# Optimization experiments

Measured on AMD Instinct MI355X. Metric: run time of the kernel, lower is better.

Reference implementation:

```python
import jax, jax.numpy as jnp
import numpy as np

N_NODES = 100000
N_EDGES = 1600000
D_FEAT = 256
HID = 128
DEG_DIM = 128  # data.degree_exist_matrix.shape[1]


def setup_inputs() -> dict:
    key = jax.random.key(0)
    ks = jax.random.split(key, 12)
    s = lambda fan_in: 1.0 / np.sqrt(fan_in)
    x = jax.random.normal(ks[0], (N_NODES, D_FEAT), dtype=jnp.float32)
    edge_index = jax.random.randint(ks[1], (2, N_EDGES), 0, N_NODES, dtype=jnp.int32)
    return {
        "x": x,
        "edge_index": edge_index,
        # GCNConv 1 / 2 (PyG stores weight [in,out], bias [out])
        "W1": jax.random.uniform(ks[2], (D_FEAT, HID), jnp.float32, -s(D_FEAT), s(D_FEAT)),
        "b1": jnp.zeros((HID,), jnp.float32),
        "W2": jax.random.uniform(ks[3], (HID, HID), jnp.float32, -s(HID), s(HID)),
        "b2": jnp.zeros((HID,), jnp.float32),
        # down_sample Linear(D_FEAT, HID)
        "Wd": jax.random.uniform(ks[4], (D_FEAT, HID), jnp.float32, -s(D_FEAT), s(D_FEAT)),
        "bd": jax.random.uniform(ks[5], (HID,), jnp.float32, -s(D_FEAT), s(D_FEAT)),
        # linear2: Degree_layer(HID, 1) ~ Linear(HID, 1)
        "Wdeg": jax.random.uniform(ks[6], (HID, 1), jnp.float32, -s(HID), s(HID)),
        "bdeg": jax.random.uniform(ks[7], (1,), jnp.float32, -s(HID), s(HID)),
        # linear3: Linear(HID, DEG_DIM)
        "W3": jax.random.uniform(ks[8], (HID, DEG_DIM), jnp.float32, -s(HID), s(HID)),
        "b3": jax.random.uniform(ks[9], (DEG_DIM,), jnp.float32, -s(HID), s(HID)),
    }


def gcn_conv(x, W, b, src, dst, n):
    """PyG GCNConv: D^-1/2 (A+I) D^-1/2 X W + b (symmetric norm, self-loops)."""
    h = x @ W  # [N, out]
    deg = jax.ops.segment_sum(jnp.ones_like(dst, dtype=h.dtype), dst, num_segments=n) + 1.0
    dinv = jax.lax.rsqrt(deg)  # deg >= 1 from self loop
    coef = dinv[src] * dinv[dst]  # [E]
    msgs = h[src] * coef[:, None]  # [E, out] -- dominant gather
    agg = jax.ops.segment_sum(msgs, dst, num_segments=n)
    agg = agg + h * (dinv * dinv)[:, None]  # self-loop contribution
    return agg + b


def reference(x, edge_index, W1, b1, W2, b2, Wd, bd, Wdeg, bdeg, W3, b3):
    n = x.shape[0]
    src, dst = edge_index[0], edge_index[1]
    original_x = x @ Wd + bd
    h = gcn_conv(x, W1, b1, src, dst, n)
    h = jax.nn.relu(h)  # dropout is identity in eval mode
    h = gcn_conv(h, W2, b2, src, dst, n)
    h = h + original_x  # residual
    result1 = jax.nn.log_softmax(h, axis=-1)        # [N, HID]
    result2 = (h @ Wdeg + bdeg).squeeze(-1)          # [N]
    result3 = h @ W3 + b3                            # [N, DEG_DIM]
    return (result1, result2, result3)
```

## Files before the change

kernel.cpp:

```cpp
#include <hip/hip_runtime.h>


typedef __attribute__((ext_vector_type(8))) short bf16x8;
typedef __attribute__((ext_vector_type(4))) float f32x4;

#define CDIV(a, b) (((a) + (b) - 1) / (b))

#define GLOBAL_AS __attribute__((address_space(1)))
#define LDS_AS __attribute__((address_space(3)))

__device__ __forceinline__ void gload16(const void* g, void* l) {
  __builtin_amdgcn_global_load_lds((const GLOBAL_AS unsigned int*)g,
                                   (LDS_AS unsigned int*)l, 16, 0, 0);
}

__device__ __forceinline__ float b2f(unsigned short u) {
  union { unsigned int i; float f; } x; x.i = ((unsigned int)u) << 16; return x.f;
}
__device__ __forceinline__ unsigned short f2b(float f) {
  union { float f; unsigned int i; } x; x.f = f;
  unsigned int r = x.i + 0x7fffu + ((x.i >> 16) & 1u);
  return (unsigned short)(r >> 16);
}
__device__ __forceinline__ float rlf(float v, int j) {
  union { float f; int i; } x; x.f = v;
  x.i = __builtin_amdgcn_readlane(x.i, j);
  return x.f;
}


__global__ void k_wtrans4(const float* __restrict__ W1, const float* __restrict__ Wd,
                          const float* __restrict__ W2, const float* __restrict__ W3,
                          unsigned short* __restrict__ W1t, unsigned short* __restrict__ Wdt,
                          unsigned short* __restrict__ W2t, unsigned short* __restrict__ W3t) {
  int idx = blockIdx.x * blockDim.x + threadIdx.x;
  const float* in; unsigned short* out; int K, N;
  if (idx < 32768)       { in = W1; out = W1t; K = 256; N = 128; }
  else if (idx < 65536)  { in = Wd; out = Wdt; K = 256; N = 128; idx -= 32768; }
  else if (idx < 81920)  { in = W2; out = W2t; K = 128; N = 128; idx -= 65536; }
  else if (idx < 98304)  { in = W3; out = W3t; K = 128; N = 128; idx -= 81920; }
  else return;
  int k = idx / N, n = idx - k * N;
  out[n * K + k] = f2b(in[idx]);
}

__global__ void k_scan1(const int* __restrict__ deg, int* __restrict__ lscan,
                        int* __restrict__ partials, float* __restrict__ dinv, int n) {
  __shared__ int sd[256];
  int tid = threadIdx.x;
  int base = blockIdx.x * 2048 + tid * 8;
  int v[8]; int tsum = 0;
#pragma unroll
  for (int i = 0; i < 8; ++i) {
    int idx = base + i;
    int xv = (idx < n) ? deg[idx] : 0;
    v[i] = xv; tsum += xv;
    if (idx < n) dinv[idx] = 1.0f / sqrtf((float)xv + 1.0f);
  }
  sd[tid] = tsum;
  __syncthreads();
  for (int off = 1; off < 256; off <<= 1) {
    int t = (tid >= off) ? sd[tid - off] : 0;
    __syncthreads();
    sd[tid] += t;
    __syncthreads();
  }
  int run = sd[tid] - tsum;
#pragma unroll
  for (int i = 0; i < 8; ++i) {
    int idx = base + i;
    if (idx < n) lscan[idx] = run;
    run += v[i];
  }
  if (tid == 255) partials[blockIdx.x] = sd[255];
}

__global__ void k_scan2(const int* __restrict__ partials, int* __restrict__ pprefix, int nb) {
  if (threadIdx.x == 0 && blockIdx.x == 0) {
    int run = 0;
    for (int i = 0; i < nb; ++i) { pprefix[i] = run; run += partials[i]; }
    pprefix[nb] = run;
  }
}

__global__ void k_scan3(const int* __restrict__ pprefix, int* row_start,
                        int* __restrict__ cursor, int n, int E) {
  int idx = blockIdx.x * blockDim.x + threadIdx.x;
  if (idx >= n) return;
  int v = row_start[idx] + pprefix[idx >> 11];
  row_start[idx] = v;
  cursor[idx] = v;
  if (idx == 0) row_start[n] = E;
}


#define BIN_CHUNK 4096
#define OVF_CAP 65536

__global__ __launch_bounds__(256) void k_binA(
    const int* __restrict__ ei, int E, int nbuck, int cap,
    int* __restrict__ deg, int2* __restrict__ pairs, int* __restrict__ bcnt,
    int2* __restrict__ ovf, int* __restrict__ ovf_cnt) {
  __shared__ int lcnt[256];
  __shared__ int lbase[256];
  int tid = threadIdx.x;
  for (int i = tid; i < nbuck; i += 256) lcnt[i] = 0;
  __syncthreads();
  int base_e = blockIdx.x * BIN_CHUNK;
  int src[16], dst[16], lofs[16];
#pragma unroll
  for (int i = 0; i < 16; ++i) {
    int e = base_e + i * 256 + tid;
    if (e < E) {
      int s = ei[e], d = ei[E + e];
      src[i] = s; dst[i] = d;
      atomicAdd(&deg[d], 1);
      lofs[i] = atomicAdd(&lcnt[d >> 9], 1);
    } else {
      dst[i] = -1;
    }
  }
  __syncthreads();
  for (int b = tid; b < nbuck; b += 256)
    lbase[b] = atomicAdd(&bcnt[b], lcnt[b]);
  __syncthreads();
#pragma unroll
  for (int i = 0; i < 16; ++i) {
    if (dst[i] < 0) continue;
    int b = dst[i] >> 9;
    int gpos = lbase[b] + lofs[i];
    if (gpos < cap) {
      pairs[(size_t)b * cap + gpos] = make_int2(src[i], dst[i]);
    } else {
      int op = atomicAdd(ovf_cnt, 1);
      if (op < OVF_CAP) ovf[op] = make_int2(src[i], dst[i]);
    }
  }
}

__global__ __launch_bounds__(256) void k_binB(
    const int2* __restrict__ pairs, const int* __restrict__ bcnt,
    int nbuck, int cap,
    const int2* __restrict__ ovf, const int* __restrict__ ovf_cnt,
    int* __restrict__ cursor, int* __restrict__ csr_src) {
  if ((int)blockIdx.x < nbuck) {
    int b = blockIdx.x;
    int cnt = bcnt[b]; if (cnt > cap) cnt = cap;
    const int2* p = pairs + (size_t)b * cap;
    for (int i = threadIdx.x; i < cnt; i += 256) {
      int2 e = p[i];
      int pos = atomicAdd(&cursor[e.y], 1);
      csr_src[pos] = e.x;
    }
  } else {
    int total = *ovf_cnt; if (total > OVF_CAP) total = OVF_CAP;
    int start = (blockIdx.x - nbuck) * 256 + threadIdx.x;
    for (int i = start; i < total; i += 8 * 256) {
      int2 e = ovf[i];
      int pos = atomicAdd(&cursor[e.y], 1);
      csr_src[pos] = e.x;
    }
  }
}


__global__ __launch_bounds__(512) void k_gemm_x2(
    const float* __restrict__ X,
    const unsigned short* __restrict__ B1t,
    const unsigned short* __restrict__ B2t,
    const float* __restrict__ bias2,
    unsigned short* __restrict__ O1, float* __restrict__ O2, int n) {
  __shared__ char lds[65536];
  const int flat = threadIdx.x;
  const int wave = flat >> 6, lane = flat & 63;
  const int l15 = lane & 15, q = lane >> 4;
  const int wM = wave >> 1, wN = wave & 1;
  const int rowBase = blockIdx.x * 128;
  const int colBase = wN * 64;

  auto stage = [&](int kb, int buf) {
    char* ldsA = lds + buf * 32768;
    char* ldsB = ldsA + 16384;
    const char* Xb = (const char*)X;
#pragma unroll
    for (int j = 0; j < 2; ++j) {
      int i = j * 512 + flat;
      int row = i >> 3, pslot = i & 7;
      int lslot = pslot ^ (row & 7);
      int rowc = rowBase + row; if (rowc >= n) rowc = n - 1;
      gload16(Xb + (size_t)rowc * 1024 + (size_t)(kb * 128 + lslot * 16),
              ldsA + (j * 512 + wave * 64) * 16);
    }
#pragma unroll
    for (int j = 0; j < 2; ++j) {
      int i = j * 512 + flat;
      int col = i >> 3, pslot = i & 7;
      int lslot = pslot ^ (col & 7);
      const char* src = (lslot >= 4) ? (const char*)B2t : (const char*)B1t;
      gload16(src + (size_t)col * 512 + kb * 64 + (lslot & 3) * 16,
              ldsB + (j * 512 + wave * 64) * 16);
    }
  };

  f32x4 acc1[2][4], acc2[2][4];
#pragma unroll
  for (int i = 0; i < 2; ++i)
#pragma unroll
    for (int j = 0; j < 4; ++j) {
      acc1[i][j] = (f32x4){0.f, 0.f, 0.f, 0.f};
      acc2[i][j] = (f32x4){0.f, 0.f, 0.f, 0.f};
    }

  stage(0, 0);
  __syncthreads();

#pragma unroll
  for (int kb = 0; kb < 8; ++kb) {
    int cur = kb & 1;
    if (kb < 7) stage(kb + 1, cur ^ 1);
    char* ldsA = lds + cur * 32768;
    char* ldsB = ldsA + 16384;
    bf16x8 a[2], b1v[4], b2v[4];
#pragma unroll
    for (int mt = 0; mt < 2; ++mt) {
      int row = wM * 32 + mt * 16 + l15;
      uint4 lo = *(const uint4*)(ldsA + row * 128 + (((2 * q) ^ (row & 7)) * 16));
      uint4 hi = *(const uint4*)(ldsA + row * 128 + (((2 * q + 1) ^ (row & 7)) * 16));
      union { bf16x8 v; unsigned int u[4]; } r;
      r.u[0] = __builtin_amdgcn_perm(lo.y + 0x8000u, lo.x + 0x8000u, 0x07060302u);
      r.u[1] = __builtin_amdgcn_perm(lo.w + 0x8000u, lo.z + 0x8000u, 0x07060302u);
      r.u[2] = __builtin_amdgcn_perm(hi.y + 0x8000u, hi.x + 0x8000u, 0x07060302u);
      r.u[3] = __builtin_amdgcn_perm(hi.w + 0x8000u, hi.z + 0x8000u, 0x07060302u);
      a[mt] = r.v;
    }
#pragma unroll
    for (int nt = 0; nt < 4; ++nt) {
      int col = colBase + nt * 16 + l15;
      b1v[nt] = *(const bf16x8*)(ldsB + col * 128 + ((q ^ (col & 7)) * 16));
      b2v[nt] = *(const bf16x8*)(ldsB + col * 128 + (((4 + q) ^ (col & 7)) * 16));
    }
#pragma unroll
    for (int mt = 0; mt < 2; ++mt)
#pragma unroll
      for (int nt = 0; nt < 4; ++nt) {
        acc1[mt][nt] = __builtin_amdgcn_mfma_f32_16x16x32_bf16(a[mt], b1v[nt], acc1[mt][nt], 0, 0, 0);
        acc2[mt][nt] = __builtin_amdgcn_mfma_f32_16x16x32_bf16(a[mt], b2v[nt], acc2[mt][nt], 0, 0, 0);
      }
    __syncthreads();
  }

#pragma unroll
  for (int mt = 0; mt < 2; ++mt)
#pragma unroll
    for (int nt = 0; nt < 4; ++nt) {
      int col = colBase + nt * 16 + l15;
      float bb = bias2[col];
#pragma unroll
      for (int r = 0; r < 4; ++r) {
        int row = rowBase + wM * 32 + mt * 16 + q * 4 + r;
        if (row < n) {
          O1[(size_t)row * 128 + col] = f2b(acc1[mt][nt][r]);
          O2[(size_t)row * 128 + col] = acc2[mt][nt][r] + bb;
        }
      }
    }
}

template <int OUT_F32>
__global__ __launch_bounds__(512) void k_gemm_h(
    const unsigned short* __restrict__ X, const unsigned short* __restrict__ Bt,
    const float* __restrict__ bias, unsigned short* __restrict__ Ob,
    float* __restrict__ Of, int n) {
  __shared__ char lds[65536];
  const int flat = threadIdx.x;
  const int wave = flat >> 6, lane = flat & 63;
  const int l15 = lane & 15, q = lane >> 4;
  const int wM = wave >> 1, wN = wave & 1;
  const int rowBase = blockIdx.x * 128;
  const int colBase = wN * 64;

  auto stage = [&](int ks, int buf) {
    char* ldsA = lds + buf * 32768;
    char* ldsB = ldsA + 16384;
#pragma unroll
    for (int j = 0; j < 2; ++j) {
      int i = j * 512 + flat;
      int row = i >> 3, pslot = i & 7;
      int lslot = pslot ^ (row & 7);
      int rowc = rowBase + row; if (rowc >= n) rowc = n - 1;
      gload16((const char*)X + (size_t)rowc * 256 + ks * 128 + lslot * 16,
              ldsA + (j * 512 + wave * 64) * 16);
    }
#pragma unroll
    for (int j = 0; j < 2; ++j) {
      int i = j * 512 + flat;
      int col = i >> 3, pslot = i & 7;
      int lslot = pslot ^ (col & 7);
      gload16((const char*)Bt + (size_t)col * 256 + ks * 128 + lslot * 16,
              ldsB + (j * 512 + wave * 64) * 16);
    }
  };

  f32x4 acc[2][4];
#pragma unroll
  for (int i = 0; i < 2; ++i)
#pragma unroll
    for (int j = 0; j < 4; ++j) acc[i][j] = (f32x4){0.f, 0.f, 0.f, 0.f};

  stage(0, 0);
  __syncthreads();
  stage(1, 1);

#pragma unroll
  for (int ks = 0; ks < 2; ++ks) {
    char* ldsA = lds + ks * 32768;
    char* ldsB = ldsA + 16384;
#pragma unroll
    for (int k2 = 0; k2 < 2; ++k2) {
      bf16x8 a[2], b[4];
#pragma unroll
      for (int mt = 0; mt < 2; ++mt) {
        int row = wM * 32 + mt * 16 + l15;
        a[mt] = *(const bf16x8*)(ldsA + row * 128 + (((k2 * 4 + q) ^ (row & 7)) * 16));
      }
#pragma unroll
      for (int nt = 0; nt < 4; ++nt) {
        int col = colBase + nt * 16 + l15;
        b[nt] = *(const bf16x8*)(ldsB + col * 128 + (((k2 * 4 + q) ^ (col & 7)) * 16));
      }
#pragma unroll
      for (int mt = 0; mt < 2; ++mt)
#pragma unroll
        for (int nt = 0; nt < 4; ++nt)
          acc[mt][nt] = __builtin_amdgcn_mfma_f32_16x16x32_bf16(a[mt], b[nt], acc[mt][nt], 0, 0, 0);
    }
    if (ks == 0) __syncthreads();
  }

#pragma unroll
  for (int mt = 0; mt < 2; ++mt)
#pragma unroll
    for (int nt = 0; nt < 4; ++nt) {
      int col = colBase + nt * 16 + l15;
      float bb = OUT_F32 ? bias[col] : 0.f;
#pragma unroll
      for (int r = 0; r < 4; ++r) {
        int row = rowBase + wM * 32 + mt * 16 + q * 4 + r;
        if (row < n) {
          if (OUT_F32) Of[(size_t)row * 128 + col] = acc[mt][nt][r] + bb;
          else Ob[(size_t)row * 128 + col] = f2b(acc[mt][nt][r]);
        }
      }
    }
}


__device__ __forceinline__ void agg_edges(
    const unsigned short* __restrict__ h, const int* __restrict__ csr_src,
    const float* __restrict__ dinv, int beg, int end, int lane,
    float& a0, float& a1) {
  for (int base = beg; base < end; base += 64) {
    int m = end - base; if (m > 64) m = 64;
    int ok = (base + lane < end);
    int idx_l = ok ? csr_src[base + lane] : 0;
    float c_l = ok ? dinv[idx_l] : 0.f;
    int j = 0;
    for (; j + 3 < m; j += 4) {
      int s0 = __builtin_amdgcn_readlane(idx_l, j);
      int s1 = __builtin_amdgcn_readlane(idx_l, j + 1);
      int s2 = __builtin_amdgcn_readlane(idx_l, j + 2);
      int s3 = __builtin_amdgcn_readlane(idx_l, j + 3);
      float c0 = rlf(c_l, j), c1 = rlf(c_l, j + 1);
      float c2 = rlf(c_l, j + 2), c3 = rlf(c_l, j + 3);
      unsigned int v0 = *(const unsigned int*)(h + (size_t)s0 * 128 + lane * 2);
      unsigned int v1 = *(const unsigned int*)(h + (size_t)s1 * 128 + lane * 2);
      unsigned int v2 = *(const unsigned int*)(h + (size_t)s2 * 128 + lane * 2);
      unsigned int v3 = *(const unsigned int*)(h + (size_t)s3 * 128 + lane * 2);
      a0 += c0 * b2f((unsigned short)v0); a1 += c0 * b2f((unsigned short)(v0 >> 16));
      a0 += c1 * b2f((unsigned short)v1); a1 += c1 * b2f((unsigned short)(v1 >> 16));
      a0 += c2 * b2f((unsigned short)v2); a1 += c2 * b2f((unsigned short)(v2 >> 16));
      a0 += c3 * b2f((unsigned short)v3); a1 += c3 * b2f((unsigned short)(v3 >> 16));
    }
    for (; j < m; ++j) {
      int s = __builtin_amdgcn_readlane(idx_l, j);
      float c = rlf(c_l, j);
      unsigned int v = *(const unsigned int*)(h + (size_t)s * 128 + lane * 2);
      a0 += c * b2f((unsigned short)v);
      a1 += c * b2f((unsigned short)(v >> 16));
    }
  }
}

__global__ __launch_bounds__(256) void k_agg1(
    const unsigned short* __restrict__ h,
    const int* __restrict__ row_start, const int* __restrict__ csr_src,
    const float* __restrict__ dinv,
    const float* __restrict__ bias,
    unsigned short* __restrict__ hout, int n) {
  int gw = blockIdx.x * (blockDim.x >> 6) + (threadIdx.x >> 6);
  int lane = threadIdx.x & 63;
  if (gw >= n) return;
  int beg = row_start[gw], end = row_start[gw + 1];
  float dg = dinv[gw];
  float a0 = 0.f, a1 = 0.f;
  agg_edges(h, csr_src, dinv, beg, end, lane, a0, a1);
  a0 *= dg; a1 *= dg;
  float sc = dg * dg;
  unsigned int v = *(const unsigned int*)(h + (size_t)gw * 128 + lane * 2);
  a0 += sc * b2f((unsigned short)v);
  a1 += sc * b2f((unsigned short)(v >> 16));
  a0 += bias[lane * 2];
  a1 += bias[lane * 2 + 1];
  a0 = fmaxf(a0, 0.f);
  a1 = fmaxf(a1, 0.f);
  unsigned int o = (unsigned int)f2b(a0) | ((unsigned int)f2b(a1) << 16);
  *(unsigned int*)(hout + (size_t)gw * 128 + lane * 2) = o;
}

__global__ __launch_bounds__(256) void k_agg2_epi(
    const unsigned short* __restrict__ h,
    const int* __restrict__ row_start, const int* __restrict__ csr_src,
    const float* __restrict__ dinv,
    const float* __restrict__ bias,
    float* res_out1,
    const float* __restrict__ wdeg, const float* __restrict__ bdeg,
    float* __restrict__ out2,
    unsigned short* __restrict__ hf,
    int n) {
  int gw = blockIdx.x * (blockDim.x >> 6) + (threadIdx.x >> 6);
  int lane = threadIdx.x & 63;
  if (gw >= n) return;
  int beg = row_start[gw], end = row_start[gw + 1];
  float dg = dinv[gw];
  float a0 = 0.f, a1 = 0.f;
  agg_edges(h, csr_src, dinv, beg, end, lane, a0, a1);
  a0 *= dg; a1 *= dg;
  float sc = dg * dg;
  unsigned int v = *(const unsigned int*)(h + (size_t)gw * 128 + lane * 2);
  a0 += sc * b2f((unsigned short)v);
  a1 += sc * b2f((unsigned short)(v >> 16));
  a0 += bias[lane * 2];
  a1 += bias[lane * 2 + 1];
  float2 rv = *(const float2*)(res_out1 + (size_t)gw * 128 + lane * 2);
  a0 += rv.x;
  a1 += rv.y;
  unsigned int o = (unsigned int)f2b(a0) | ((unsigned int)f2b(a1) << 16);
  *(unsigned int*)(hf + (size_t)gw * 128 + lane * 2) = o;
  float t = a0 * wdeg[lane * 2] + a1 * wdeg[lane * 2 + 1];
#pragma unroll
  for (int m = 32; m >= 1; m >>= 1) t += __shfl_xor(t, m);
  if (lane == 0) out2[gw] = t + bdeg[0];
  float mx = fmaxf(a0, a1);
#pragma unroll
  for (int m = 32; m >= 1; m >>= 1) mx = fmaxf(mx, __shfl_xor(mx, m));
  float l = __expf(a0 - mx) + __expf(a1 - mx);
#pragma unroll
  for (int m = 32; m >= 1; m >>= 1) l += __shfl_xor(l, m);
  float ls = mx + __logf(l);
  float2 o1; o1.x = a0 - ls; o1.y = a1 - ls;
  *(float2*)(res_out1 + (size_t)gw * 128 + lane * 2) = o1;
}


extern "C" void kernel_launch(void* const* d_in, const int* in_sizes, int n_in,
                              void* d_out, int out_size, void* d_ws, size_t ws_size,
                              hipStream_t stream) {
  const float* x   = (const float*)d_in[0];
  const int*   ei  = (const int*)d_in[1];
  const float* W1  = (const float*)d_in[2];
  const float* b1  = (const float*)d_in[3];
  const float* W2  = (const float*)d_in[4];
  const float* b2  = (const float*)d_in[5];
  const float* Wd  = (const float*)d_in[6];
  const float* bd  = (const float*)d_in[7];
  const float* Wdg = (const float*)d_in[8];
  const float* bdg = (const float*)d_in[9];
  const float* W3  = (const float*)d_in[10];
  const float* b3  = (const float*)d_in[11];

  const int N = in_sizes[0] / 256;
  const int E = in_sizes[1] / 2;

  char* w = (char*)d_ws;
  auto alloc = [&](size_t bytes) {
    char* p = w;
    w += (bytes + 255) & ~(size_t)255;
    return p;
  };
  unsigned short* W1t  = (unsigned short*)alloc((size_t)256 * 128 * 2);
  unsigned short* Wdt  = (unsigned short*)alloc((size_t)256 * 128 * 2);
  unsigned short* W2t  = (unsigned short*)alloc((size_t)128 * 128 * 2);
  unsigned short* W3t  = (unsigned short*)alloc((size_t)128 * 128 * 2);
  unsigned short* bufC = (unsigned short*)alloc((size_t)N * 128 * 2);
  int*   deg      = (int*)alloc((size_t)N * 4);
  float* dinv     = (float*)alloc((size_t)N * 4);
  int*   row_start= (int*)alloc((size_t)(N + 1) * 4);
  int*   cursor   = (int*)alloc((size_t)N * 4);
  int*   partials = (int*)alloc(4096);
  int*   pprefix  = (int*)alloc(4096);
  int*   csr_src  = (int*)alloc((size_t)E * 4);
  int*   bcnt     = (int*)alloc(2048);
  int*   ovf_cnt  = bcnt + 256;
  int2*  ovf      = (int2*)alloc((size_t)OVF_CAP * 8);

  float* out1 = (float*)d_out;
  float* out2 = out1 + (size_t)N * 128;
  float* out3 = out2 + (size_t)N;
  unsigned short* bufA = (unsigned short*)out3;

  const int nbuck = CDIV(N, 512);
  int cap = (E / nbuck) + (E / nbuck) / 2;
  cap = (cap + 255) & ~255;
  size_t bufC_bytes = (size_t)N * 128 * 2;
  if ((size_t)nbuck * cap * 8 > bufC_bytes)
    cap = (int)(bufC_bytes / ((size_t)nbuck * 8));
  int2* pairs = (int2*)bufC;

  hipMemsetAsync(deg, 0, (size_t)N * 4, stream);
  hipMemsetAsync(bcnt, 0, 2048, stream);

  k_wtrans4<<<CDIV(98304, 256), 256, 0, stream>>>(W1, Wd, W2, W3, W1t, Wdt, W2t, W3t);

  k_binA<<<CDIV(E, BIN_CHUNK), 256, 0, stream>>>(ei, E, nbuck, cap, deg, pairs,
                                                 bcnt, ovf, ovf_cnt);

  k_gemm_x2<<<CDIV(N, 128), 512, 0, stream>>>(x, W1t, Wdt, bd, bufA, out1, N);

  const int nb = CDIV(N, 2048);
  k_scan1<<<nb, 256, 0, stream>>>(deg, row_start, partials, dinv, N);
  k_scan2<<<1, 64, 0, stream>>>(partials, pprefix, nb);
  k_scan3<<<CDIV(N, 256), 256, 0, stream>>>(pprefix, row_start, cursor, N, E);

  k_binB<<<nbuck + 8, 256, 0, stream>>>(pairs, bcnt, nbuck, cap, ovf, ovf_cnt,
                                        cursor, csr_src);

  k_agg1<<<CDIV(N, 4), 256, 0, stream>>>(bufA, row_start, csr_src, dinv, b1, bufC, N);

  k_gemm_h<0><<<CDIV(N, 128), 512, 0, stream>>>(bufC, W2t, nullptr, bufA, nullptr, N);

  k_agg2_epi<<<CDIV(N, 4), 256, 0, stream>>>(bufA, row_start, csr_src, dinv,
                                             b2, out1, Wdg, bdg, out2, bufC, N);

  k_gemm_h<1><<<CDIV(N, 128), 512, 0, stream>>>(bufC, W3t, b3, nullptr, out3, N);
}
```

Baseline: 534.7 us.

## Pre-scale GEMM outputs by dinv and gather edges with 16-byte loads

The source-side normalisation dinv[src] is folded into the GEMM epilogues, so the aggregation kernels gather pre-scaled rows and only add them. This removes the per-edge dinv gather and multiply. The edge loop now splits a wave into four 16-lane groups, each loading a full 256-byte row with uint4 loads on a different edge, then reduces across groups with shuffles. The first GEMM moves after the degree scan so dinv exists when it runs, which removes its overlap with the scan. The change also adds nontemporal stores and a cheaper bf16 pack, and pads dinv so the float4 reads past N stay in bounds.

```diff
diff --git a/kernel.cpp b/kernel.cpp
--- a/kernel.cpp
+++ b/kernel.cpp
@@ -22,10 +22,14 @@
   unsigned int r = x.i + 0x7fffu + ((x.i >> 16) & 1u);
   return (unsigned short)(r >> 16);
 }
-__device__ __forceinline__ float rlf(float v, int j) {
-  union { float f; int i; } x; x.f = v;
-  x.i = __builtin_amdgcn_readlane(x.i, j);
-  return x.f;
+__device__ __forceinline__ void add2(float& a0, float& a1, unsigned int u) {
+  union { unsigned int i; float f; } lo, hi;
+  lo.i = u << 16; hi.i = u & 0xffff0000u;
+  a0 += lo.f; a1 += hi.f;
+}
+__device__ __forceinline__ unsigned int pack2(float lo, float hi) {
+  return __builtin_amdgcn_perm(__float_as_uint(hi) + 0x8000u,
+                               __float_as_uint(lo) + 0x8000u, 0x07060302u);
 }
 
 
@@ -169,6 +173,7 @@
     const unsigned short* __restrict__ B1t,
     const unsigned short* __restrict__ B2t,
     const float* __restrict__ bias2,
+    const float* __restrict__ dinvp,
     unsigned short* __restrict__ O1, float* __restrict__ O2, int n) {
   __shared__ char lds[65536];
   const int flat = threadIdx.x;
@@ -250,7 +255,8 @@
   }
 
 #pragma unroll
-  for (int mt = 0; mt < 2; ++mt)
+  for (int mt = 0; mt < 2; ++mt) {
+    float4 dv = *(const float4*)(dinvp + rowBase + wM * 32 + mt * 16 + q * 4);
 #pragma unroll
     for (int nt = 0; nt < 4; ++nt) {
       int col = colBase + nt * 16 + l15;
@@ -259,18 +265,20 @@
       for (int r = 0; r < 4; ++r) {
         int row = rowBase + wM * 32 + mt * 16 + q * 4 + r;
         if (row < n) {
-          O1[(size_t)row * 128 + col] = f2b(acc1[mt][nt][r]);
+          float dvr = (r == 0) ? dv.x : (r == 1) ? dv.y : (r == 2) ? dv.z : dv.w;
+          O1[(size_t)row * 128 + col] = f2b(acc1[mt][nt][r] * dvr);
           O2[(size_t)row * 128 + col] = acc2[mt][nt][r] + bb;
         }
       }
     }
+  }
 }
 
 template <int OUT_F32>
 __global__ __launch_bounds__(512) void k_gemm_h(
     const unsigned short* __restrict__ X, const unsigned short* __restrict__ Bt,
-    const float* __restrict__ bias, unsigned short* __restrict__ Ob,
-    float* __restrict__ Of, int n) {
+    const float* __restrict__ bias, const float* __restrict__ dinvp,
+    unsigned short* __restrict__ Ob, float* __restrict__ Of, int n) {
   __shared__ char lds[65536];
   const int flat = threadIdx.x;
   const int wave = flat >> 6, lane = flat & 63;
@@ -338,7 +346,9 @@
   }
 
 #pragma unroll
-  for (int mt = 0; mt < 2; ++mt)
+  for (int mt = 0; mt < 2; ++mt) {
+    float4 dv;
+    if (!OUT_F32) dv = *(const float4*)(dinvp + rowBase + wM * 32 + mt * 16 + q * 4);
 #pragma unroll
     for (int nt = 0; nt < 4; ++nt) {
       int col = colBase + nt * 16 + l15;
@@ -347,47 +357,59 @@
       for (int r = 0; r < 4; ++r) {
         int row = rowBase + wM * 32 + mt * 16 + q * 4 + r;
         if (row < n) {
-          if (OUT_F32) Of[(size_t)row * 128 + col] = acc[mt][nt][r] + bb;
-          else Ob[(size_t)row * 128 + col] = f2b(acc[mt][nt][r]);
+          if (OUT_F32) {
+            __builtin_nontemporal_store(acc[mt][nt][r] + bb, &Of[(size_t)row * 128 + col]);
+          } else {
+            float dvr = (r == 0) ? dv.x : (r == 1) ? dv.y : (r == 2) ? dv.z : dv.w;
+            Ob[(size_t)row * 128 + col] = f2b(acc[mt][nt][r] * dvr);
+          }
         }
       }
     }
-}
-
-
-__device__ __forceinline__ void agg_edges(
+  }
+}
+
+
+__device__ __forceinline__ void agg_edges4(
     const unsigned short* __restrict__ h, const int* __restrict__ csr_src,
-    const float* __restrict__ dinv, int beg, int end, int lane,
-    float& a0, float& a1) {
+    int beg, int end, int lane, int grp, int sub, float* acc) {
   for (int base = beg; base < end; base += 64) {
     int m = end - base; if (m > 64) m = 64;
-    int ok = (base + lane < end);
-    int idx_l = ok ? csr_src[base + lane] : 0;
-    float c_l = ok ? dinv[idx_l] : 0.f;
-    int j = 0;
-    for (; j + 3 < m; j += 4) {
-      int s0 = __builtin_amdgcn_readlane(idx_l, j);
-      int s1 = __builtin_amdgcn_readlane(idx_l, j + 1);
-      int s2 = __builtin_amdgcn_readlane(idx_l, j + 2);
-      int s3 = __builtin_amdgcn_readlane(idx_l, j + 3);
-      float c0 = rlf(c_l, j), c1 = rlf(c_l, j + 1);
-      float c2 = rlf(c_l, j + 2), c3 = rlf(c_l, j + 3);
-      unsigned int v0 = *(const unsigned int*)(h + (size_t)s0 * 128 + lane * 2);
-      unsigned int v1 = *(const unsigned int*)(h + (size_t)s1 * 128 + lane * 2);
-      unsigned int v2 = *(const unsigned int*)(h + (size_t)s2 * 128 + lane * 2);
-      unsigned int v3 = *(const unsigned int*)(h + (size_t)s3 * 128 + lane * 2);
-      a0 += c0 * b2f((unsigned short)v0); a1 += c0 * b2f((unsigned short)(v0 >> 16));
-      a0 += c1 * b2f((unsigned short)v1); a1 += c1 * b2f((unsigned short)(v1 >> 16));
-      a0 += c2 * b2f((unsigned short)v2); a1 += c2 * b2f((unsigned short)(v2 >> 16));
-      a0 += c3 * b2f((unsigned short)v3); a1 += c3 * b2f((unsigned short)(v3 >> 16));
-    }
-    for (; j < m; ++j) {
-      int s = __builtin_amdgcn_readlane(idx_l, j);
-      float c = rlf(c_l, j);
-      unsigned int v = *(const unsigned int*)(h + (size_t)s * 128 + lane * 2);
-      a0 += c * b2f((unsigned short)v);
-      a1 += c * b2f((unsigned short)(v >> 16));
-    }
+    int idx_l = (base + lane < end) ? csr_src[base + lane] : 0;
+    for (int j = 0; j < m; j += 16) {
+      int s0 = __builtin_amdgcn_ds_bpermute((j + grp) << 2, idx_l);
+      int s1 = __builtin_amdgcn_ds_bpermute((j + 4 + grp) << 2, idx_l);
+      int s2 = __builtin_amdgcn_ds_bpermute((j + 8 + grp) << 2, idx_l);
+      int s3 = __builtin_amdgcn_ds_bpermute((j + 12 + grp) << 2, idx_l);
+      uint4 v0 = *(const uint4*)(h + (size_t)s0 * 128 + sub * 8);
+      uint4 v1 = *(const uint4*)(h + (size_t)s1 * 128 + sub * 8);
+      uint4 v2 = *(const uint4*)(h + (size_t)s2 * 128 + sub * 8);
+      uint4 v3 = *(const uint4*)(h + (size_t)s3 * 128 + sub * 8);
+      if (j + grp < m) {
+        add2(acc[0], acc[1], v0.x); add2(acc[2], acc[3], v0.y);
+        add2(acc[4], acc[5], v0.z); add2(acc[6], acc[7], v0.w);
+      }
+      if (j + 4 + grp < m) {
+        add2(acc[0], acc[1], v1.x); add2(acc[2], acc[3], v1.y);
+        add2(acc[4], acc[5], v1.z); add2(acc[6], acc[7], v1.w);
+      }
+      if (j + 8 + grp < m) {
+        add2(acc[0], acc[1], v2.x); add2(acc[2], acc[3], v2.y);
+        add2(acc[4], acc[5], v2.z); add2(acc[6], acc[7], v2.w);
+      }
+      if (j + 12 + grp < m) {
+        add2(acc[0], acc[1], v3.x); add2(acc[2], acc[3], v3.y);
+        add2(acc[4], acc[5], v3.z); add2(acc[6], acc[7], v3.w);
+      }
+    }
+  }
+}
+
+__device__ __forceinline__ void grp_reduce(float* acc) {
+#pragma unroll
+  for (int i = 0; i < 8; ++i) {
+    acc[i] += __shfl_xor(acc[i], 16);
+    acc[i] += __shfl_xor(acc[i], 32);
   }
 }
 
@@ -397,24 +419,31 @@
     const float* __restrict__ dinv,
     const float* __restrict__ bias,
     unsigned short* __restrict__ hout, int n) {
-  int gw = blockIdx.x * (blockDim.x >> 6) + (threadIdx.x >> 6);
+  int gw = blockIdx.x * 4 + (threadIdx.x >> 6);
   int lane = threadIdx.x & 63;
+  int grp = lane >> 4, sub = lane & 15;
   if (gw >= n) return;
   int beg = row_start[gw], end = row_start[gw + 1];
-  float dg = dinv[gw];
-  float a0 = 0.f, a1 = 0.f;
-  agg_edges(h, csr_src, dinv, beg, end, lane, a0, a1);
-  a0 *= dg; a1 *= dg;
-  float sc = dg * dg;
-  unsigned int v = *(const unsigned int*)(h + (size_t)gw * 128 + lane * 2);
-  a0 += sc * b2f((unsigned short)v);
-  a1 += sc * b2f((unsigned short)(v >> 16));
-  a0 += bias[lane * 2];
-  a1 += bias[lane * 2 + 1];
-  a0 = fmaxf(a0, 0.f);
-  a1 = fmaxf(a1, 0.f);
-  unsigned int o = (unsigned int)f2b(a0) | ((unsigned int)f2b(a1) << 16);
-  *(unsigned int*)(hout + (size_t)gw * 128 + lane * 2) = o;
+  float acc[8] = {0.f, 0.f, 0.f, 0.f, 0.f, 0.f, 0.f, 0.f};
+  agg_edges4(h, csr_src, beg, end, lane, grp, sub, acc);
+  grp_reduce(acc);
+  if (grp == 0) {
+    float dg = dinv[gw];
+    uint4 sv = *(const uint4*)(h + (size_t)gw * 128 + sub * 8);
+    add2(acc[0], acc[1], sv.x); add2(acc[2], acc[3], sv.y);
+    add2(acc[4], acc[5], sv.z); add2(acc[6], acc[7], sv.w);
+    float4 b0 = *(const float4*)(bias + sub * 8);
+    float4 b1v = *(const float4*)(bias + sub * 8 + 4);
+    float a[8];
+    a[0] = fmaxf(acc[0] * dg + b0.x, 0.f); a[1] = fmaxf(acc[1] * dg + b0.y, 0.f);
+    a[2] = fmaxf(acc[2] * dg + b0.z, 0.f); a[3] = fmaxf(acc[3] * dg + b0.w, 0.f);
+    a[4] = fmaxf(acc[4] * dg + b1v.x, 0.f); a[5] = fmaxf(acc[5] * dg + b1v.y, 0.f);
+    a[6] = fmaxf(acc[6] * dg + b1v.z, 0.f); a[7] = fmaxf(acc[7] * dg + b1v.w, 0.f);
+    uint4 o;
+    o.x = pack2(a[0], a[1]); o.y = pack2(a[2], a[3]);
+    o.z = pack2(a[4], a[5]); o.w = pack2(a[6], a[7]);
+    *(uint4*)(hout + (size_t)gw * 128 + sub * 8) = o;
+  }
 }
 
 __global__ __launch_bounds__(256) void k_agg2_epi(
@@ -427,38 +456,55 @@
     float* __restrict__ out2,
     unsigned short* __restrict__ hf,
     int n) {
-  int gw = blockIdx.x * (blockDim.x >> 6) + (threadIdx.x >> 6);
+  int gw = blockIdx.x * 4 + (threadIdx.x >> 6);
   int lane = threadIdx.x & 63;
+  int grp = lane >> 4, sub = lane & 15;
   if (gw >= n) return;
   int beg = row_start[gw], end = row_start[gw + 1];
-  float dg = dinv[gw];
-  float a0 = 0.f, a1 = 0.f;
-  agg_edges(h, csr_src, dinv, beg, end, lane, a0, a1);
-  a0 *= dg; a1 *= dg;
-  float sc = dg * dg;
-  unsigned int v = *(const unsigned int*)(h + (size_t)gw * 128 + lane * 2);
-  a0 += sc * b2f((unsigned short)v);
-  a1 += sc * b2f((unsigned short)(v >> 16));
-  a0 += bias[lane * 2];
-  a1 += bias[lane * 2 + 1];
-  float2 rv = *(const float2*)(res_out1 + (size_t)gw * 128 + lane * 2);
-  a0 += rv.x;
-  a1 += rv.y;
-  unsigned int o = (unsigned int)f2b(a0) | ((unsigned int)f2b(a1) << 16);
-  *(unsigned int*)(hf + (size_t)gw * 128 + lane * 2) = o;
-  float t = a0 * wdeg[lane * 2] + a1 * wdeg[lane * 2 + 1];
-#pragma unroll
-  for (int m = 32; m >= 1; m >>= 1) t += __shfl_xor(t, m);
-  if (lane == 0) out2[gw] = t + bdeg[0];
-  float mx = fmaxf(a0, a1);
-#pragma unroll
-  for (int m = 32; m >= 1; m >>= 1) mx = fmaxf(mx, __shfl_xor(mx, m));
-  float l = __expf(a0 - mx) + __expf(a1 - mx);
-#pragma unroll
-  for (int m = 32; m >= 1; m >>= 1) l += __shfl_xor(l, m);
-  float ls = mx + __logf(l);
-  float2 o1; o1.x = a0 - ls; o1.y = a1 - ls;
-  *(float2*)(res_out1 + (size_t)gw * 128 + lane * 2) = o1;
+  float acc[8] = {0.f, 0.f, 0.f, 0.f, 0.f, 0.f, 0.f, 0.f};
+  agg_edges4(h, csr_src, beg, end, lane, grp, sub, acc);
+  grp_reduce(acc);
+  if (grp == 0) {
+    float dg = dinv[gw];
+    uint4 sv = *(const uint4*)(h + (size_t)gw * 128 + sub * 8);
+    add2(acc[0], acc[1], sv.x); add2(acc[2], acc[3], sv.y);
+    add2(acc[4], acc[5], sv.z); add2(acc[6], acc[7], sv.w);
+    float4 b0 = *(const float4*)(bias + sub * 8);
+    float4 b1v = *(const float4*)(bias + sub * 8 + 4);
+    float4 r0 = *(const float4*)(res_out1 + (size_t)gw * 128 + sub * 8);
+    float4 r1 = *(const float4*)(res_out1 + (size_t)gw * 128 + sub * 8 + 4);
+    float a[8];
+    a[0] = acc[0] * dg + b0.x + r0.x; a[1] = acc[1] * dg + b0.y + r0.y;
+    a[2] = acc[2] * dg + b0.z + r0.z; a[3] = acc[3] * dg + b0.w + r0.w;
+    a[4] = acc[4] * dg + b1v.x + r1.x; a[5] = acc[5] * dg + b1v.y + r1.y;
+    a[6] = acc[6] * dg + b1v.z + r1.z; a[7] = acc[7] * dg + b1v.w + r1.w;
+    uint4 o;
+    o.x = pack2(a[0], a[1]); o.y = pack2(a[2], a[3]);
+    o.z = pack2(a[4], a[5]); o.w = pack2(a[6], a[7]);
+    *(uint4*)(hf + (size_t)gw * 128 + sub * 8) = o;
+    float4 w0 = *(const float4*)(wdeg + sub * 8);
+    float4 w1 = *(const float4*)(wdeg + sub * 8 + 4);
+    float t = a[0] * w0.x + a[1] * w0.y + a[2] * w0.z + a[3] * w0.w +
+              a[4] * w1.x + a[5] * w1.y + a[6] * w1.z + a[7] * w1.w;
+#pragma unroll
+    for (int mk = 8; mk >= 1; mk >>= 1) t += __shfl_xor(t, mk);
+    if (sub == 0) __builtin_nontemporal_store(t + bdeg[0], out2 + gw);
+    float mx = a[0];
+#pragma unroll
+    for (int i = 1; i < 8; ++i) mx = fmaxf(mx, a[i]);
+#pragma unroll
+    for (int mk = 8; mk >= 1; mk >>= 1) mx = fmaxf(mx, __shfl_xor(mx, mk));
+    float l = 0.f;
+#pragma unroll
+    for (int i = 0; i < 8; ++i) l += __expf(a[i] - mx);
+#pragma unroll
+    for (int mk = 8; mk >= 1; mk >>= 1) l += __shfl_xor(l, mk);
+    float ls = mx + __logf(l);
+    f32x4 o0 = {a[0] - ls, a[1] - ls, a[2] - ls, a[3] - ls};
+    f32x4 o1 = {a[4] - ls, a[5] - ls, a[6] - ls, a[7] - ls};
+    __builtin_nontemporal_store(o0, (f32x4*)(res_out1 + (size_t)gw * 128 + sub * 8));
+    __builtin_nontemporal_store(o1, (f32x4*)(res_out1 + (size_t)gw * 128 + sub * 8 + 4));
+  }
 }
 
 
@@ -493,7 +539,7 @@
   unsigned short* W3t  = (unsigned short*)alloc((size_t)128 * 128 * 2);
   unsigned short* bufC = (unsigned short*)alloc((size_t)N * 128 * 2);
   int*   deg      = (int*)alloc((size_t)N * 4);
-  float* dinv     = (float*)alloc((size_t)N * 4);
+  float* dinv     = (float*)alloc((size_t)(N + 128) * 4);
   int*   row_start= (int*)alloc((size_t)(N + 1) * 4);
   int*   cursor   = (int*)alloc((size_t)N * 4);
   int*   partials = (int*)alloc(4096);
@@ -524,22 +570,22 @@
   k_binA<<<CDIV(E, BIN_CHUNK), 256, 0, stream>>>(ei, E, nbuck, cap, deg, pairs,
                                                  bcnt, ovf, ovf_cnt);
 
-  k_gemm_x2<<<CDIV(N, 128), 512, 0, stream>>>(x, W1t, Wdt, bd, bufA, out1, N);
-
   const int nb = CDIV(N, 2048);
   k_scan1<<<nb, 256, 0, stream>>>(deg, row_start, partials, dinv, N);
   k_scan2<<<1, 64, 0, stream>>>(partials, pprefix, nb);
   k_scan3<<<CDIV(N, 256), 256, 0, stream>>>(pprefix, row_start, cursor, N, E);
 
+  k_gemm_x2<<<CDIV(N, 128), 512, 0, stream>>>(x, W1t, Wdt, bd, dinv, bufA, out1, N);
+
   k_binB<<<nbuck + 8, 256, 0, stream>>>(pairs, bcnt, nbuck, cap, ovf, ovf_cnt,
                                         cursor, csr_src);
 
   k_agg1<<<CDIV(N, 4), 256, 0, stream>>>(bufA, row_start, csr_src, dinv, b1, bufC, N);
 
-  k_gemm_h<0><<<CDIV(N, 128), 512, 0, stream>>>(bufC, W2t, nullptr, bufA, nullptr, N);
+  k_gemm_h<0><<<CDIV(N, 128), 512, 0, stream>>>(bufC, W2t, nullptr, dinv, bufA, nullptr, N);
 
   k_agg2_epi<<<CDIV(N, 4), 256, 0, stream>>>(bufA, row_start, csr_src, dinv,
                                              b2, out1, Wdg, bdg, out2, bufC, N);
 
-  k_gemm_h<1><<<CDIV(N, 128), 512, 0, stream>>>(bufC, W3t, b3, nullptr, out3, N);
-}
+  k_gemm_h<1><<<CDIV(N, 128), 512, 0, stream>>>(bufC, W3t, b3, nullptr, nullptr, out3, N);
+}
```

Measured after the change: 533.0 us. No clear change (-0.3%).
